# Optimization experiments

Measured on AMD Instinct MI355X. Metric: run time of the kernel, lower is better.

## Reference

```python
import jax, jax.numpy as jnp
import numpy as np

N_HEADS = 16

def _ln(x, g, b, eps=1e-5):
    m = jnp.mean(x, axis=-1, keepdims=True)
    v = jnp.mean((x - m) ** 2, axis=-1, keepdims=True)
    return (x - m) / jnp.sqrt(v + eps) * g + b

def _gelu(x):
    return jax.nn.gelu(x, approximate=False)

def _forward(x, pos_embed, time_embed, Wint, bint, g1, be1, Wq, bq, Wk, bk, Wv, bv,
             Wo, bo, Wm1, bm1, Wm2, bm2, g2, be2, W5, b5, ew, g3, be3, Wf1, bf1, Wf2, bf2):
    B, T, C = x.shape
    H = N_HEADS
    dh = C // H
    # PositionTimingLayer: concat pos/time halves, linear, residual add
    fused = jnp.concatenate([pos_embed[:T], time_embed[:T]], axis=-1)  # [T, C]
    x = x + fused @ Wint.T + bint
    # MechanismAttention on norm1(x)
    h = _ln(x, g1, be1)
    q = (h @ Wq.T + bq).reshape(B, T, H, dh)
    k = (h @ Wk.T + bk).reshape(B, T, H, dh)
    v = (h @ Wv.T + bv).reshape(B, T, H, dh)
    scores = jnp.einsum('bthd,bshd->bhts', q, k) / np.float32(np.sqrt(dh))  # [B,H,T,T]
    mech = jax.nn.sigmoid(_gelu(h @ Wm1.T + bm1) @ Wm2.T + bm2)[..., 0]  # [B,T]
    scores = scores * (1.0 + mech[:, None, None, :])  # modulate along key dim
    attn = jax.nn.softmax(scores, axis=-1)
    ctx = jnp.einsum('bhts,bshd->bthd', attn, v).reshape(B, T, C)
    x = x + (ctx @ Wo.T + bo)
    # FiveElementsTransformationLayer on norm2(x)
    h2 = _ln(x, g2, be2)
    proj = jnp.einsum('bti,eoi->bteo', h2, W5) + b5  # [B,T,5,C]
    w = jax.nn.softmax(ew)
    x = x + jnp.einsum('e,bteo->bto', w, proj)
    # FFN on norm3(x)
    h3 = _ln(x, g3, be3)
    x = x + (_gelu(h3 @ Wf1.T + bf1) @ Wf2.T + bf2)
    return x, mech, w

def setup_inputs() -> dict:
    key = jax.random.key(0)
    d, dff, L, five = 1024, 4096, 1024, 5
    ks = jax.random.split(key, 32)
    s = 0.02
    r = lambda i, shape: jax.random.normal(ks[i], shape, dtype=jnp.float32) * s
    return {
        'x': jax.random.normal(ks[0], (4, L, d), dtype=jnp.float32),
        'pos_embed': r(1, (L, d // 2)), 'time_embed': r(2, (L, d // 2)),
        'Wint': r(3, (d, d)), 'bint': jnp.zeros((d,)),
        'g1': jnp.ones((d,)), 'be1': jnp.zeros((d,)),
        'Wq': r(4, (d, d)), 'bq': jnp.zeros((d,)),
        'Wk': r(5, (d, d)), 'bk': jnp.zeros((d,)),
        'Wv': r(6, (d, d)), 'bv': jnp.zeros((d,)),
        'Wo': r(7, (d, d)), 'bo': jnp.zeros((d,)),
        'Wm1': r(8, (d // 2, d)), 'bm1': jnp.zeros((d // 2,)),
        'Wm2': r(9, (1, d // 2)), 'bm2': jnp.zeros((1,)),
        'g2': jnp.ones((d,)), 'be2': jnp.zeros((d,)),
        'W5': r(10, (five, d, d)), 'b5': jnp.zeros((five, d)),
        'ew': jnp.ones((five,)) / five,
        'g3': jnp.ones((d,)), 'be3': jnp.zeros((d,)),
        'Wf1': r(11, (dff, d)), 'bf1': jnp.zeros((dff,)),
        'Wf2': r(12, (d, dff)), 'bf2': jnp.zeros((d,)),
    }

def reference(x, pos_embed, time_embed, Wint, bint, g1, be1, Wq, bq, Wk, bk, Wv, bv,
              Wo, bo, Wm1, bm1, Wm2, bm2, g2, be2, W5, b5, ew, g3, be3, Wf1, bf1, Wf2, bf2):
    return _forward(x, pos_embed, time_embed, Wint, bint, g1, be1, Wq, bq, Wk, bk, Wv, bv,
                    Wo, bo, Wm1, bm1, Wm2, bm2, g2, be2, W5, b5, ew, g3, be3, Wf1, bf1, Wf2, bf2)
```

## Files before the change

kernel.cpp:

```cpp
#include <hip/hip_runtime.h>

typedef unsigned short u16;
typedef __bf16 bf16_t;
typedef bf16_t bf16x8 __attribute__((ext_vector_type(8)));
typedef bf16_t bf16x4 __attribute__((ext_vector_type(4)));
typedef float f32x4 __attribute__((ext_vector_type(4)));

__device__ __forceinline__ u16 f2b(float f){
  unsigned u = __builtin_bit_cast(unsigned, f);
  u += 0x7fffu + ((u >> 16) & 1u);
  return (u16)(u >> 16);
}
__device__ __forceinline__ float b2f(u16 h){
  return __builtin_bit_cast(float, ((unsigned)h) << 16);
}
__device__ __forceinline__ float gelu_exact(float x){
  return 0.5f * x * (1.f + erff(x * 0.70710678118654752440f));
}
__device__ __forceinline__ void gld16(const void* g, void* l){
  __builtin_amdgcn_global_load_lds((const __attribute__((address_space(1))) unsigned int*)g,
                                   (__attribute__((address_space(3))) unsigned int*)l, 16, 0, 0);
}

__global__ void k_conv(const float* __restrict__ s, u16* __restrict__ d, int n){
  int i = (blockIdx.x * 256 + threadIdx.x) * 4;
  if (i >= n) return;
  float4 v = *(const float4*)(s + i);
  ushort4 o; o.x = f2b(v.x); o.y = f2b(v.y); o.z = f2b(v.z); o.w = f2b(v.w);
  *(ushort4*)(d + i) = o;
}

__global__ void k_w5(const float* __restrict__ W5, const float* __restrict__ b5,
                     const float* __restrict__ ew, u16* __restrict__ Wc,
                     float* __restrict__ b5c, float* __restrict__ outW){
  int gid = blockIdx.x * 256 + threadIdx.x;
  float e0 = ew[0], e1 = ew[1], e2 = ew[2], e3 = ew[3], e4 = ew[4];
  float mx = fmaxf(fmaxf(fmaxf(e0, e1), fmaxf(e2, e3)), e4);
  float x0 = __expf(e0 - mx), x1 = __expf(e1 - mx), x2 = __expf(e2 - mx), x3 = __expf(e3 - mx), x4 = __expf(e4 - mx);
  float inv = 1.f / (x0 + x1 + x2 + x3 + x4);
  float w0 = x0 * inv, w1 = x1 * inv, w2 = x2 * inv, w3 = x3 * inv, w4 = x4 * inv;
  float v = w0 * W5[gid] + w1 * W5[gid + 1048576] + w2 * W5[gid + 2097152]
          + w3 * W5[gid + 3145728] + w4 * W5[gid + 4194304];
  Wc[gid] = f2b(v);
  if (gid < 1024)
    b5c[gid] = w0 * b5[gid] + w1 * b5[gid + 1024] + w2 * b5[gid + 2048]
             + w3 * b5[gid + 3072] + w4 * b5[gid + 4096];
  if (gid == 0){ outW[0] = w0; outW[1] = w1; outW[2] = w2; outW[3] = w3; outW[4] = w4; }
}

__global__ void k_fused(const float* __restrict__ pos, const float* __restrict__ tim,
                        u16* __restrict__ d){
  int i = blockIdx.x * 256 + threadIdx.x;
  int t = i >> 10, c = i & 1023;
  float v = (c < 512) ? pos[t * 512 + c] : tim[t * 512 + c - 512];
  d[i] = f2b(v);
}

__global__ void k_bqkv(const float* __restrict__ bq, const float* __restrict__ bk,
                       const float* __restrict__ bv, float* __restrict__ d){
  int i = blockIdx.x * 256 + threadIdx.x;
  if (i >= 3072) return;
  d[i] = (i < 1024) ? bq[i] : (i < 2048 ? bk[i - 1024] : bv[i - 2048]);
}

__global__ void k_xinit(const float* __restrict__ xin, const float* __restrict__ tmp,
                        float* __restrict__ x){
  int i = blockIdx.x * 256 + threadIdx.x;
  float4 a = ((const float4*)xin)[i];
  float4 b = ((const float4*)tmp)[i & 262143];
  float4 o; o.x = a.x + b.x; o.y = a.y + b.y; o.z = a.z + b.z; o.w = a.w + b.w;
  ((float4*)x)[i] = o;
}

__global__ __launch_bounds__(256) void k_ln(const float* __restrict__ x, const float* __restrict__ g,
                     const float* __restrict__ be, u16* __restrict__ out){
  int row = blockIdx.x, tid = threadIdx.x;
  int w = tid >> 6, lane = tid & 63;
  const float4 v = ((const float4*)(x + (size_t)row * 1024))[tid];
  float s1 = v.x + v.y + v.z + v.w;
  float s2 = v.x * v.x + v.y * v.y + v.z * v.z + v.w * v.w;
  for (int m = 1; m < 64; m <<= 1){ s1 += __shfl_xor(s1, m, 64); s2 += __shfl_xor(s2, m, 64); }
  __shared__ float a1[4], a2[4];
  if (!lane){ a1[w] = s1; a2[w] = s2; }
  __syncthreads();
  s1 = a1[0] + a1[1] + a1[2] + a1[3];
  s2 = a2[0] + a2[1] + a2[2] + a2[3];
  float mean = s1 * (1.f / 1024.f);
  float var  = s2 * (1.f / 1024.f) - mean * mean;
  float rstd = rsqrtf(var + 1e-5f);
  float4 gv = ((const float4*)g)[tid], bv = ((const float4*)be)[tid];
  ushort4 o;
  o.x = f2b((v.x - mean) * rstd * gv.x + bv.x);
  o.y = f2b((v.y - mean) * rstd * gv.y + bv.y);
  o.z = f2b((v.z - mean) * rstd * gv.z + bv.z);
  o.w = f2b((v.w - mean) * rstd * gv.w + bv.w);
  ((ushort4*)(out + (size_t)row * 1024))[tid] = o;
}

__global__ __launch_bounds__(256) void k_mech(const u16* __restrict__ m1, const float* __restrict__ Wm2,
                      const float* __restrict__ bm2, float* __restrict__ outMech,
                      float* __restrict__ mechf){
  int tid = threadIdx.x, w = tid >> 6, lane = tid & 63;
  int r = blockIdx.x * 4 + w;
  uint4 mv = *(const uint4*)(m1 + (size_t)r * 512 + lane * 8);
  const u16* ms = (const u16*)&mv;
  float4 w0 = ((const float4*)Wm2)[lane * 2];
  float4 w1 = ((const float4*)Wm2)[lane * 2 + 1];
  float dot = b2f(ms[0]) * w0.x + b2f(ms[1]) * w0.y + b2f(ms[2]) * w0.z + b2f(ms[3]) * w0.w
            + b2f(ms[4]) * w1.x + b2f(ms[5]) * w1.y + b2f(ms[6]) * w1.z + b2f(ms[7]) * w1.w;
  for (int m = 1; m < 64; m <<= 1) dot += __shfl_xor(dot, m, 64);
  if (lane == 0){
    float z = dot + bm2[0];
    float sig = 1.f / (1.f + __expf(-z));
    outMech[r] = sig;
    mechf[r] = (1.f + sig) * 0.125f;
  }
}

__global__ __launch_bounds__(256) void k_vt(const u16* __restrict__ qkv, u16* __restrict__ vT){
  __shared__ u16 lt[64 * 64];
  const int tid = threadIdx.x;
  const int b = blockIdx.z, h = blockIdx.y, t0 = blockIdx.x * 64;
  const size_t base = (size_t)b * 1024;
#pragma unroll
  for (int i = 0; i < 2; ++i){
    int c = i * 256 + tid;
    int r = c >> 3, ch = c & 7;
    uint4 v = *(const uint4*)(qkv + (base + t0 + r) * 3072 + 2048 + h * 64 + ch * 8);
    *(uint4*)((char*)lt + r * 128 + ((ch ^ (r & 7)) << 4)) = v;
  }
  __syncthreads();
  int d = tid >> 2, tt = (tid & 3) * 16;
  u16 o[16];
#pragma unroll
  for (int j = 0; j < 16; ++j){
    int t = tt + j;
    o[j] = *(const u16*)((char*)lt + t * 128 + (((d >> 3) ^ (t & 7)) << 4) + (d & 7) * 2);
  }
  u16* dst = vT + ((size_t)(b * 16 + h) * 64 + d) * 1024 + t0 + tt;
  *(uint4*)dst = *(uint4*)&o[0];
  *(uint4*)(dst + 8) = *(uint4*)&o[8];
}

template<bool GELU_, bool RES, bool OUTF_EN, bool OUTB_EN>
__global__ __launch_bounds__(256) void k_gemm(const u16* __restrict__ A, const u16* __restrict__ W,
                      const float* __restrict__ bias, const float* resid,
                      float* outF, u16* outB, int M, int N, int K){
  __shared__ u16 lA[128 * 32];
  __shared__ u16 lB[128 * 32];
  const int tid = threadIdx.x;
  const int w = tid >> 6, lane = tid & 63;
  const int lr = lane & 15, lg = lane >> 4;
  const int m0 = blockIdx.y * 128, n0 = blockIdx.x * 128;
  const int wr = (w >> 1) * 64, wc = (w & 1) * 64;

  f32x4 acc[4][4] = {};
  const char* gA = (const char*)A;
  const char* gW = (const char*)W;

  for (int k0 = 0; k0 < K; k0 += 32){
    __syncthreads();
#pragma unroll
    for (int i = 0; i < 2; ++i){
      int c = i * 256 + tid;
      gld16(gA + (((size_t)(m0 + (c >> 2)) * K + k0) * 2 + (c & 3) * 16),
            (char*)lA + i * 4096 + w * 1024);
      gld16(gW + (((size_t)(n0 + (c >> 2)) * K + k0) * 2 + (c & 3) * 16),
            (char*)lB + i * 4096 + w * 1024);
    }
    __syncthreads();
    bf16x8 af[4], wf[4];
#pragma unroll
    for (int mb = 0; mb < 4; ++mb)
      af[mb] = *reinterpret_cast<const bf16x8*>(&lA[(wr + mb * 16 + lr) * 32 + lg * 8]);
#pragma unroll
    for (int nb = 0; nb < 4; ++nb)
      wf[nb] = *reinterpret_cast<const bf16x8*>(&lB[(wc + nb * 16 + lr) * 32 + lg * 8]);
#pragma unroll
    for (int mb = 0; mb < 4; ++mb)
#pragma unroll
      for (int nb = 0; nb < 4; ++nb)
        acc[mb][nb] = __builtin_amdgcn_mfma_f32_16x16x32_bf16(af[mb], wf[nb], acc[mb][nb], 0, 0, 0);
  }

#pragma unroll
  for (int mb = 0; mb < 4; ++mb){
#pragma unroll
    for (int nb = 0; nb < 4; ++nb){
      int col = n0 + wc + nb * 16 + lr;
      float bv = bias[col];
#pragma unroll
      for (int ii = 0; ii < 4; ++ii){
        int row = m0 + wr + mb * 16 + lg * 4 + ii;
        float v = acc[mb][nb][ii] + bv;
        if (GELU_) v = gelu_exact(v);
        size_t idx = (size_t)row * N + col;
        if (RES) v += resid[idx];
        if (OUTF_EN) outF[idx] = v;
        if (OUTB_EN) outB[idx] = f2b(v);
      }
    }
  }
}

__global__ __launch_bounds__(256) void k_attn(const u16* __restrict__ qkv, const u16* __restrict__ vT,
                      const float* __restrict__ mechf, u16* __restrict__ ctx){
  __shared__ u16 lk[64 * 64];
  __shared__ u16 lvt[64 * 64];
  __shared__ u16 lpt[4][64 * 16];
  __shared__ float lmf[64];
  const int tid = threadIdx.x, w = tid >> 6, lane = tid & 63;
  const int lr = lane & 15, lg = lane >> 4;
  const int b = blockIdx.z, h = blockIdx.y, q0 = blockIdx.x * 64;
  const size_t base = (size_t)b * 1024;
  const size_t bh = (size_t)(b * 16 + h);

  bf16x8 qf[2];
  {
    const u16* qrow = qkv + (base + q0 + w * 16 + lr) * 3072 + h * 64;
    qf[0] = *(const bf16x8*)(qrow + lg * 8);
    qf[1] = *(const bf16x8*)(qrow + 32 + lg * 8);
  }
  float m_i[4], l_i[4];
  f32x4 cacc[4] = {};
#pragma unroll
  for (int i = 0; i < 4; ++i){ m_i[i] = -1e30f; l_i[i] = 0.f; }

  char* lkb = (char*)lk;
  char* lvb = (char*)lvt;
  unsigned lpw = (unsigned)(uintptr_t)(__attribute__((address_space(3))) u16*)&lpt[w][0];
  unsigned ta = lpw + lg * 256 + lr * 8;

  for (int jt = 0; jt < 1024; jt += 64){
    __syncthreads();
#pragma unroll
    for (int i = 0; i < 2; ++i){
      int c = i * 256 + tid;
      int row = c >> 3, ch = c & 7;
      int chs = ch ^ (row & 7);
      gld16(qkv + (base + jt + row) * 3072 + 1024 + h * 64 + chs * 8,
            lkb + i * 4096 + w * 1024);
      gld16(vT + (bh * 64 + row) * 1024 + jt + chs * 8,
            lvb + i * 4096 + w * 1024);
    }
    if (tid < 64) lmf[tid] = mechf[base + jt + tid];
    __syncthreads();

    f32x4 s[4];
    __builtin_amdgcn_s_setprio(1);
#pragma unroll
    for (int kb = 0; kb < 4; ++kb){
      int row = kb * 16 + lr;
      bf16x8 kf0 = *(const bf16x8*)(lkb + row * 128 + ((lg ^ (row & 7)) << 4));
      bf16x8 kf1 = *(const bf16x8*)(lkb + row * 128 + (((4 + lg) ^ (row & 7)) << 4));
      f32x4 z = {};
      z = __builtin_amdgcn_mfma_f32_16x16x32_bf16(qf[0], kf0, z, 0, 0, 0);
      z = __builtin_amdgcn_mfma_f32_16x16x32_bf16(qf[1], kf1, z, 0, 0, 0);
      float f = lmf[row];
      s[kb] = z * f;
    }
    __builtin_amdgcn_s_setprio(0);

    float tm[4];
#pragma unroll
    for (int i = 0; i < 4; ++i)
      tm[i] = fmaxf(fmaxf(s[0][i], s[1][i]), fmaxf(s[2][i], s[3][i]));
#pragma unroll
    for (int off = 1; off < 16; off <<= 1)
#pragma unroll
      for (int i = 0; i < 4; ++i) tm[i] = fmaxf(tm[i], __shfl_xor(tm[i], off, 64));
    float sc[4];
#pragma unroll
    for (int i = 0; i < 4; ++i){
      float mn = fmaxf(m_i[i], tm[i]);
      sc[i] = __expf(m_i[i] - mn);
      m_i[i] = mn;
    }
#pragma unroll
    for (int kb = 0; kb < 4; ++kb){
      ushort4 pk;
      float p0 = __expf(s[kb][0] - m_i[0]); s[kb][0] = p0; pk.x = f2b(p0);
      float p1 = __expf(s[kb][1] - m_i[1]); s[kb][1] = p1; pk.y = f2b(p1);
      float p2 = __expf(s[kb][2] - m_i[2]); s[kb][2] = p2; pk.z = f2b(p2);
      float p3 = __expf(s[kb][3] - m_i[3]); s[kb][3] = p3; pk.w = f2b(p3);
      *(uint2*)((char*)&lpt[w][0] + (kb * 16 + lr) * 32 + lg * 8) =
          __builtin_bit_cast(uint2, pk);
    }
#pragma unroll
    for (int i = 0; i < 4; ++i){
      float r = (s[0][i] + s[1][i]) + (s[2][i] + s[3][i]);
#pragma unroll
      for (int off = 1; off < 16; off <<= 1) r += __shfl_xor(r, off, 64);
      l_i[i] = l_i[i] * sc[i] + r;
#pragma unroll
      for (int db = 0; db < 4; ++db) cacc[db][i] *= sc[i];
    }

    asm volatile("s_waitcnt lgkmcnt(0)" ::: "memory");
    bf16x4 t00, t01, t10, t11;
    asm volatile("ds_read_b64_tr_b16 %0, %1 offset:0"    : "=v"(t00) : "v"(ta));
    asm volatile("ds_read_b64_tr_b16 %0, %1 offset:128"  : "=v"(t01) : "v"(ta));
    asm volatile("ds_read_b64_tr_b16 %0, %1 offset:1024" : "=v"(t10) : "v"(ta));
    asm volatile("ds_read_b64_tr_b16 %0, %1 offset:1152" : "=v"(t11) : "v"(ta));
    asm volatile("s_waitcnt lgkmcnt(0)");
    __builtin_amdgcn_sched_barrier(0);
    bf16x8 pf0 = __builtin_shufflevector(t00, t01, 0, 1, 2, 3, 4, 5, 6, 7);
    bf16x8 pf1 = __builtin_shufflevector(t10, t11, 0, 1, 2, 3, 4, 5, 6, 7);

    __builtin_amdgcn_s_setprio(1);
#pragma unroll
    for (int db = 0; db < 4; ++db){
      int row = db * 16 + lr;
      bf16x8 vf0 = *(const bf16x8*)(lvb + row * 128 + ((lg ^ (row & 7)) << 4));
      bf16x8 vf1 = *(const bf16x8*)(lvb + row * 128 + (((4 + lg) ^ (row & 7)) << 4));
      cacc[db] = __builtin_amdgcn_mfma_f32_16x16x32_bf16(pf0, vf0, cacc[db], 0, 0, 0);
      cacc[db] = __builtin_amdgcn_mfma_f32_16x16x32_bf16(pf1, vf1, cacc[db], 0, 0, 0);
    }
    __builtin_amdgcn_s_setprio(0);
  }
  size_t orow0 = base + q0 + w * 16;
#pragma unroll
  for (int db = 0; db < 4; ++db)
#pragma unroll
    for (int i = 0; i < 4; ++i)
      ctx[(orow0 + lg * 4 + i) * 1024 + h * 64 + db * 16 + lr] = f2b(cacc[db][i] / l_i[i]);
}

extern "C" void kernel_launch(void* const* d_in, const int* in_sizes, int n_in,
                              void* d_out, int out_size, void* d_ws, size_t ws_size,
                              hipStream_t stream){
  const float* x_in = (const float*)d_in[0];
  const float* pos  = (const float*)d_in[1];
  const float* tim  = (const float*)d_in[2];
  const float* Wint = (const float*)d_in[3];
  const float* bint = (const float*)d_in[4];
  const float* g1   = (const float*)d_in[5];
  const float* be1  = (const float*)d_in[6];
  const float* Wq   = (const float*)d_in[7];
  const float* bq   = (const float*)d_in[8];
  const float* Wk   = (const float*)d_in[9];
  const float* bk   = (const float*)d_in[10];
  const float* Wv   = (const float*)d_in[11];
  const float* bv   = (const float*)d_in[12];
  const float* Wo   = (const float*)d_in[13];
  const float* bo   = (const float*)d_in[14];
  const float* Wm1  = (const float*)d_in[15];
  const float* bm1  = (const float*)d_in[16];
  const float* Wm2  = (const float*)d_in[17];
  const float* bm2  = (const float*)d_in[18];
  const float* g2   = (const float*)d_in[19];
  const float* be2  = (const float*)d_in[20];
  const float* W5   = (const float*)d_in[21];
  const float* b5   = (const float*)d_in[22];
  const float* ew   = (const float*)d_in[23];
  const float* g3   = (const float*)d_in[24];
  const float* be3  = (const float*)d_in[25];
  const float* Wf1  = (const float*)d_in[26];
  const float* bf1  = (const float*)d_in[27];
  const float* Wf2  = (const float*)d_in[28];
  const float* bf2  = (const float*)d_in[29];

  float* outX = (float*)d_out;
  float* outM = outX + 4194304;
  float* outW = outX + 4198400;

  char* p = (char*)d_ws;
  auto alloc = [&](size_t bytes) -> char* {
    char* r = p; p += (bytes + 255) & ~(size_t)255; return r;
  };
  u16* Wint_b = (u16*)alloc(1048576 * 2);
  u16* Wqkv_b = (u16*)alloc(3145728 * 2);
  u16* Wm1_b  = (u16*)alloc(524288 * 2);
  u16* Wo_b   = (u16*)alloc(1048576 * 2);
  u16* Wc_b   = (u16*)alloc(1048576 * 2);
  u16* Wf1_b  = (u16*)alloc(4194304 * 2);
  u16* Wf2_b  = (u16*)alloc(4194304 * 2);
  u16* fus_b  = (u16*)alloc(1048576 * 2);
  float* bqkv = (float*)alloc(3072 * 4);
  float* b5c  = (float*)alloc(1024 * 4);
  float* mechf= (float*)alloc(4096 * 4);
  float* tmpF = (float*)alloc(1048576 * 4);
  float* xbuf = (float*)alloc(4194304 * 4);
  u16* h_b    = (u16*)alloc(4194304 * 2);
  char* big   = alloc(36 * 1024 * 1024);
  u16* qkv_b  = (u16*)big;
  u16* m1_b   = (u16*)(big + 24 * 1024 * 1024);
  u16* ctx_b  = (u16*)(big + 28 * 1024 * 1024);
  u16* f1_b   = (u16*)big;
  u16* vT_b   = h_b;

  dim3 blk(256);
  k_conv<<<1024, blk, 0, stream>>>(Wint, Wint_b, 1048576);
  k_conv<<<1024, blk, 0, stream>>>(Wq, Wqkv_b, 1048576);
  k_conv<<<1024, blk, 0, stream>>>(Wk, Wqkv_b + 1048576, 1048576);
  k_conv<<<1024, blk, 0, stream>>>(Wv, Wqkv_b + 2097152, 1048576);
  k_conv<<<512,  blk, 0, stream>>>(Wm1, Wm1_b, 524288);
  k_conv<<<1024, blk, 0, stream>>>(Wo, Wo_b, 1048576);
  k_conv<<<4096, blk, 0, stream>>>(Wf1, Wf1_b, 4194304);
  k_conv<<<4096, blk, 0, stream>>>(Wf2, Wf2_b, 4194304);
  k_w5<<<4096, blk, 0, stream>>>(W5, b5, ew, Wc_b, b5c, outW);
  k_fused<<<4096, blk, 0, stream>>>(pos, tim, fus_b);
  k_bqkv<<<12, blk, 0, stream>>>(bq, bk, bv, bqkv);

  k_gemm<false,false,true,false><<<dim3(8, 8), blk, 0, stream>>>(
      fus_b, Wint_b, bint, nullptr, tmpF, nullptr, 1024, 1024, 1024);
  k_xinit<<<4096, blk, 0, stream>>>(x_in, tmpF, xbuf);

  k_ln<<<4096, blk, 0, stream>>>(xbuf, g1, be1, h_b);
  k_gemm<false,false,false,true><<<dim3(24, 32), blk, 0, stream>>>(
      h_b, Wqkv_b, bqkv, nullptr, nullptr, qkv_b, 4096, 3072, 1024);
  k_gemm<true,false,false,true><<<dim3(4, 32), blk, 0, stream>>>(
      h_b, Wm1_b, bm1, nullptr, nullptr, m1_b, 4096, 512, 1024);
  k_mech<<<1024, blk, 0, stream>>>(m1_b, Wm2, bm2, outM, mechf);
  k_vt<<<dim3(16, 16, 4), blk, 0, stream>>>(qkv_b, vT_b);
  k_attn<<<dim3(16, 16, 4), blk, 0, stream>>>(qkv_b, vT_b, mechf, ctx_b);
  k_gemm<false,true,true,false><<<dim3(8, 32), blk, 0, stream>>>(
      ctx_b, Wo_b, bo, xbuf, xbuf, nullptr, 4096, 1024, 1024);

  k_ln<<<4096, blk, 0, stream>>>(xbuf, g2, be2, h_b);
  k_gemm<false,true,true,false><<<dim3(8, 32), blk, 0, stream>>>(
      h_b, Wc_b, b5c, xbuf, xbuf, nullptr, 4096, 1024, 1024);

  k_ln<<<4096, blk, 0, stream>>>(xbuf, g3, be3, h_b);
  k_gemm<true,false,false,true><<<dim3(32, 32), blk, 0, stream>>>(
      h_b, Wf1_b, bf1, nullptr, nullptr, f1_b, 4096, 4096, 1024);
  k_gemm<false,true,true,false><<<dim3(8, 32), blk, 0, stream>>>(
      f1_b, Wf2_b, bf2, xbuf, outX, nullptr, 4096, 1024, 4096);
}
```

Baseline: 621.2 us.

## Double-buffer GEMM LDS, add XCD-aware block swizzle, split-K the FFN down-projection

The GEMM kernel now double-buffers its LDS tiles so the global-to-LDS load of the next K step overlaps the MFMA work on the current one, with one barrier per iteration. Blocks are launched on a 1D grid and remapped so consecutive tiles land on the same XCD, aiming to improve L2 reuse. The final FFN GEMM (K=4096) is split into two K halves that write bf16 partial sums, then a new reduction kernel adds the partials, bias and residual. The split doubles the block count for that GEMM but costs an extra pass over memory and rounds the partials to bf16, which lowers precision.

After: 574.4 us. 7.5% less time.

```diff
diff --git a/kernel.cpp b/kernel.cpp
--- a/kernel.cpp
+++ b/kernel.cpp
@@ -142,45 +142,60 @@
   *(uint4*)(dst + 8) = *(uint4*)&o[8];
 }
 
-template<bool GELU_, bool RES, bool OUTF_EN, bool OUTB_EN>
+template<bool GELU_, bool RES, bool OUTF_EN, bool OUTB_EN, bool PARTIAL>
 __global__ __launch_bounds__(256) void k_gemm(const u16* __restrict__ A, const u16* __restrict__ W,
                       const float* __restrict__ bias, const float* resid,
-                      float* outF, u16* outB, int M, int N, int K){
-  __shared__ u16 lA[128 * 32];
-  __shared__ u16 lB[128 * 32];
+                      float* outF, u16* outB, u16* pOut, int M, int N, int K, int nbx){
+  __shared__ u16 lA[2][128 * 32];
+  __shared__ u16 lB[2][128 * 32];
   const int tid = threadIdx.x;
   const int w = tid >> 6, lane = tid & 63;
   const int lr = lane & 15, lg = lane >> 4;
-  const int m0 = blockIdx.y * 128, n0 = blockIdx.x * 128;
+  const int nwg = gridDim.x;
+  const int q = nwg >> 3, r = nwg & 7;
+  const int xcd = blockIdx.x & 7, loc = blockIdx.x >> 3;
+  const int swz = (xcd < r ? xcd * (q + 1) : r * (q + 1) + (xcd - r) * q) + loc;
+  const int m0 = (swz / nbx) * 128, n0 = (swz % nbx) * 128;
   const int wr = (w >> 1) * 64, wc = (w & 1) * 64;
+  const int kb = blockIdx.z;
+  const int Ks = K / gridDim.z;
+  const int kbeg = kb * Ks;
+  const int nsteps = Ks >> 5;
 
   f32x4 acc[4][4] = {};
   const char* gA = (const char*)A;
   const char* gW = (const char*)W;
 
-  for (int k0 = 0; k0 < K; k0 += 32){
-    __syncthreads();
+  auto stage = [&](int buf, int k0){
 #pragma unroll
     for (int i = 0; i < 2; ++i){
       int c = i * 256 + tid;
       gld16(gA + (((size_t)(m0 + (c >> 2)) * K + k0) * 2 + (c & 3) * 16),
-            (char*)lA + i * 4096 + w * 1024);
+            (char*)lA + buf * 8192 + i * 4096 + w * 1024);
       gld16(gW + (((size_t)(n0 + (c >> 2)) * K + k0) * 2 + (c & 3) * 16),
-            (char*)lB + i * 4096 + w * 1024);
-    }
-    __syncthreads();
+            (char*)lB + buf * 8192 + i * 4096 + w * 1024);
+    }
+  };
+
+  stage(0, kbeg);
+  __syncthreads();
+  int cur = 0;
+  for (int s = 0; s < nsteps; ++s){
+    if (s + 1 < nsteps) stage(cur ^ 1, kbeg + (s + 1) * 32);
     bf16x8 af[4], wf[4];
 #pragma unroll
     for (int mb = 0; mb < 4; ++mb)
-      af[mb] = *reinterpret_cast<const bf16x8*>(&lA[(wr + mb * 16 + lr) * 32 + lg * 8]);
+      af[mb] = *reinterpret_cast<const bf16x8*>(&lA[cur][(wr + mb * 16 + lr) * 32 + lg * 8]);
 #pragma unroll
     for (int nb = 0; nb < 4; ++nb)
-      wf[nb] = *reinterpret_cast<const bf16x8*>(&lB[(wc + nb * 16 + lr) * 32 + lg * 8]);
+      wf[nb] = *reinterpret_cast<const bf16x8*>(&lB[cur][(wc + nb * 16 + lr) * 32 + lg * 8]);
 #pragma unroll
     for (int mb = 0; mb < 4; ++mb)
 #pragma unroll
       for (int nb = 0; nb < 4; ++nb)
         acc[mb][nb] = __builtin_amdgcn_mfma_f32_16x16x32_bf16(af[mb], wf[nb], acc[mb][nb], 0, 0, 0);
+    __syncthreads();
+    cur ^= 1;
   }
 
 #pragma unroll
@@ -188,7 +203,7 @@
 #pragma unroll
     for (int nb = 0; nb < 4; ++nb){
       int col = n0 + wc + nb * 16 + lr;
-      float bv = bias[col];
+      float bv = PARTIAL ? 0.f : bias[col];
 #pragma unroll
       for (int ii = 0; ii < 4; ++ii){
         int row = m0 + wr + mb * 16 + lg * 4 + ii;
@@ -196,11 +211,37 @@
         if (GELU_) v = gelu_exact(v);
         size_t idx = (size_t)row * N + col;
         if (RES) v += resid[idx];
+        if (PARTIAL) pOut[(size_t)kb * M * N + idx] = f2b(v);
         if (OUTF_EN) outF[idx] = v;
         if (OUTB_EN) outB[idx] = f2b(v);
       }
     }
   }
+}
+
+__global__ __launch_bounds__(256) void k_red(const u16* __restrict__ pw, const float* __restrict__ bias,
+                     const float* __restrict__ resid, float* __restrict__ outF, int MN, int N){
+  int i = (blockIdx.x * 256 + threadIdx.x) * 8;
+  uint4 v0 = *(const uint4*)(pw + i);
+  uint4 v1 = *(const uint4*)(pw + MN + i);
+  const u16* a = (const u16*)&v0;
+  const u16* b = (const u16*)&v1;
+  int col = i & (N - 1);
+  float4 bv0 = *(const float4*)(bias + col);
+  float4 bv1 = *(const float4*)(bias + col + 4);
+  float4 r0 = *(const float4*)(resid + i);
+  float4 r1 = *(const float4*)(resid + i + 4);
+  float4 o0, o1;
+  o0.x = b2f(a[0]) + b2f(b[0]) + bv0.x + r0.x;
+  o0.y = b2f(a[1]) + b2f(b[1]) + bv0.y + r0.y;
+  o0.z = b2f(a[2]) + b2f(b[2]) + bv0.z + r0.z;
+  o0.w = b2f(a[3]) + b2f(b[3]) + bv0.w + r0.w;
+  o1.x = b2f(a[4]) + b2f(b[4]) + bv1.x + r1.x;
+  o1.y = b2f(a[5]) + b2f(b[5]) + bv1.y + r1.y;
+  o1.z = b2f(a[6]) + b2f(b[6]) + bv1.z + r1.z;
+  o1.w = b2f(a[7]) + b2f(b[7]) + bv1.w + r1.w;
+  *(float4*)(outF + i) = o0;
+  *(float4*)(outF + i + 4) = o1;
 }
 
 __global__ __launch_bounds__(256) void k_attn(const u16* __restrict__ qkv, const u16* __restrict__ vT,
@@ -388,6 +429,7 @@
   u16* ctx_b  = (u16*)(big + 28 * 1024 * 1024);
   u16* f1_b   = (u16*)big;
   u16* vT_b   = h_b;
+  u16* pw_b   = (u16*)d_ws;
 
   dim3 blk(256);
   k_conv<<<1024, blk, 0, stream>>>(Wint, Wint_b, 1048576);
@@ -402,28 +444,29 @@
   k_fused<<<4096, blk, 0, stream>>>(pos, tim, fus_b);
   k_bqkv<<<12, blk, 0, stream>>>(bq, bk, bv, bqkv);
 
-  k_gemm<false,false,true,false><<<dim3(8, 8), blk, 0, stream>>>(
-      fus_b, Wint_b, bint, nullptr, tmpF, nullptr, 1024, 1024, 1024);
+  k_gemm<false,false,true,false,false><<<dim3(64, 1, 1), blk, 0, stream>>>(
+      fus_b, Wint_b, bint, nullptr, tmpF, nullptr, nullptr, 1024, 1024, 1024, 8);
   k_xinit<<<4096, blk, 0, stream>>>(x_in, tmpF, xbuf);
 
   k_ln<<<4096, blk, 0, stream>>>(xbuf, g1, be1, h_b);
-  k_gemm<false,false,false,true><<<dim3(24, 32), blk, 0, stream>>>(
-      h_b, Wqkv_b, bqkv, nullptr, nullptr, qkv_b, 4096, 3072, 1024);
-  k_gemm<true,false,false,true><<<dim3(4, 32), blk, 0, stream>>>(
-      h_b, Wm1_b, bm1, nullptr, nullptr, m1_b, 4096, 512, 1024);
+  k_gemm<false,false,false,true,false><<<dim3(768, 1, 1), blk, 0, stream>>>(
+      h_b, Wqkv_b, bqkv, nullptr, nullptr, qkv_b, nullptr, 4096, 3072, 1024, 24);
+  k_gemm<true,false,false,true,false><<<dim3(128, 1, 1), blk, 0, stream>>>(
+      h_b, Wm1_b, bm1, nullptr, nullptr, m1_b, nullptr, 4096, 512, 1024, 4);
   k_mech<<<1024, blk, 0, stream>>>(m1_b, Wm2, bm2, outM, mechf);
   k_vt<<<dim3(16, 16, 4), blk, 0, stream>>>(qkv_b, vT_b);
   k_attn<<<dim3(16, 16, 4), blk, 0, stream>>>(qkv_b, vT_b, mechf, ctx_b);
-  k_gemm<false,true,true,false><<<dim3(8, 32), blk, 0, stream>>>(
-      ctx_b, Wo_b, bo, xbuf, xbuf, nullptr, 4096, 1024, 1024);
+  k_gemm<false,true,true,false,false><<<dim3(256, 1, 1), blk, 0, stream>>>(
+      ctx_b, Wo_b, bo, xbuf, xbuf, nullptr, nullptr, 4096, 1024, 1024, 8);
 
   k_ln<<<4096, blk, 0, stream>>>(xbuf, g2, be2, h_b);
-  k_gemm<false,true,true,false><<<dim3(8, 32), blk, 0, stream>>>(
-      h_b, Wc_b, b5c, xbuf, xbuf, nullptr, 4096, 1024, 1024);
+  k_gemm<false,true,true,false,false><<<dim3(256, 1, 1), blk, 0, stream>>>(
+      h_b, Wc_b, b5c, xbuf, xbuf, nullptr, nullptr, 4096, 1024, 1024, 8);
 
   k_ln<<<4096, blk, 0, stream>>>(xbuf, g3, be3, h_b);
-  k_gemm<true,false,false,true><<<dim3(32, 32), blk, 0, stream>>>(
-      h_b, Wf1_b, bf1, nullptr, nullptr, f1_b, 4096, 4096, 1024);
-  k_gemm<false,true,true,false><<<dim3(8, 32), blk, 0, stream>>>(
-      f1_b, Wf2_b, bf2, xbuf, outX, nullptr, 4096, 1024, 4096);
-}
+  k_gemm<true,false,false,true,false><<<dim3(1024, 1, 1), blk, 0, stream>>>(
+      h_b, Wf1_b, bf1, nullptr, nullptr, f1_b, nullptr, 4096, 4096, 1024, 32);
+  k_gemm<false,false,false,false,true><<<dim3(256, 1, 2), blk, 0, stream>>>(
+      f1_b, Wf2_b, nullptr, nullptr, nullptr, nullptr, pw_b, 4096, 1024, 4096, 8);
+  k_red<<<2048, blk, 0, stream>>>(pw_b, bf2, xbuf, outX, 4194304, 1024);
+}
```
